# Kernel tuning notes

Hardware: AMD Instinct MI355X
Metric: run time of the kernel (lower is better)

## Reference

```python
import jax, jax.numpy as jnp
import numpy as np

N_NODES = 100000
N_EDGES = 1600000
NEG_SLOPE = 0.01  # F.leaky_relu default


def _param(key, shape, scale=0.05):
    return jax.random.normal(key, shape, dtype=jnp.float32) * scale


def setup_inputs() -> dict:
    key = jax.random.key(0)
    ks = jax.random.split(key, 32)
    inp = {
        "x": jax.random.normal(ks[0], (N_NODES, 64), dtype=jnp.float32),
        "edge_index": jax.random.randint(ks[1], (2, N_EDGES), 0, N_NODES, dtype=jnp.int64),
        # encoder SAGEConv params: lin_l (neighbors, with bias) + lin_r (root)
        "ggn1_Wl": _param(ks[2], (128, 64)), "ggn1_b": jnp.zeros((128,), jnp.float32), "ggn1_Wr": _param(ks[3], (128, 64)),
        "ggn2_Wl": _param(ks[4], (128, 128)), "ggn2_b": jnp.zeros((128,), jnp.float32), "ggn2_Wr": _param(ks[5], (128, 128)),
        "ggn3_Wl": _param(ks[6], (128, 128)), "ggn3_b": jnp.zeros((128,), jnp.float32), "ggn3_Wr": _param(ks[7], (128, 128)),
        "tr2_W": _param(ks[8], (64, 128)), "tr2_b": jnp.zeros((64,), jnp.float32),
        # decoder
        "dec1_W": _param(ks[9], (128, 64)), "dec1_b": jnp.zeros((128,), jnp.float32),
        "dec2_Wl": _param(ks[10], (128, 128)), "dec2_b": jnp.zeros((128,), jnp.float32), "dec2_Wr": _param(ks[11], (128, 128)),
        "dec3_Wl": _param(ks[12], (64, 128)), "dec3_b": jnp.zeros((64,), jnp.float32), "dec3_Wr": _param(ks[13], (64, 128)),
        "dec4_Wl": _param(ks[14], (3, 64)), "dec4_b": jnp.zeros((3,), jnp.float32), "dec4_Wr": _param(ks[15], (3, 64)),
    }
    return inp


def _sage(x, src, dst, Wl, b, Wr, n):
    # PyG SAGEConv (aggr='mean'): lin_l(mean_{j->i} x_j) + lin_r(x_i)
    msgs = x[src]                                              # [E, d] gather
    s = jax.ops.segment_sum(msgs, dst, num_segments=n)          # [N, d]
    cnt = jax.ops.segment_sum(jnp.ones((src.shape[0], 1), x.dtype), dst, num_segments=n)
    mean = s / jnp.maximum(cnt, 1.0)
    return mean @ Wl.T + b + x @ Wr.T


def _leaky(h):
    return jnp.where(h > 0, h, NEG_SLOPE * h)


def reference(x, edge_index,
              ggn1_Wl, ggn1_b, ggn1_Wr,
              ggn2_Wl, ggn2_b, ggn2_Wr,
              ggn3_Wl, ggn3_b, ggn3_Wr,
              tr2_W, tr2_b,
              dec1_W, dec1_b,
              dec2_Wl, dec2_b, dec2_Wr,
              dec3_Wl, dec3_b, dec3_Wr,
              dec4_Wl, dec4_b, dec4_Wr):
    n = x.shape[0]
    src, dst = edge_index[0], edge_index[1]  # source_to_target flow
    # --- encode (dropout = identity, deterministic reference) ---
    h = jnp.tanh(_sage(x, src, dst, ggn1_Wl, ggn1_b, ggn1_Wr, n))
    h = jnp.tanh(_sage(h, src, dst, ggn2_Wl, ggn2_b, ggn2_Wr, n))
    h = jnp.tanh(_sage(h, src, dst, ggn3_Wl, ggn3_b, ggn3_Wr, n))
    mu = h @ tr2_W.T + tr2_b
    logvar = mu  # module applies the same tr2 twice
    z = mu       # reparametrize in eval mode returns mu
    # --- decode ---
    o = _leaky(z @ dec1_W.T + dec1_b)
    o = _leaky(_sage(o, src, dst, dec2_Wl, dec2_b, dec2_Wr, n))
    o = jnp.tanh(_sage(o, src, dst, dec3_Wl, dec3_b, dec3_Wr, n))
    z2 = _sage(o, src, dst, dec4_Wl, dec4_b, dec4_Wr, n)
    return (z2[:, :2], z2[:, 2], mu, logvar)
```

## Files before the change

### kernel.cpp

```cpp
#include <hip/hip_runtime.h>
#include <cmath>


constexpr int ACT_NONE = 0, ACT_TANH = 1, ACT_LEAKY = 2;
constexpr int SCAN_CHUNK = 4096;

typedef __attribute__((ext_vector_type(8))) __bf16 bf16x8;
typedef __attribute__((ext_vector_type(4))) float f32x4;
typedef __attribute__((ext_vector_type(4))) unsigned short u16x4;
typedef __attribute__((ext_vector_type(8))) unsigned short u16x8;

__device__ __forceinline__ unsigned short f2h(float x) {
  _Float16 h = (_Float16)x;
  unsigned short u;
  __builtin_memcpy(&u, &h, 2);
  return u;
}
__device__ __forceinline__ float hlo(unsigned int u) {
  unsigned short s = (unsigned short)(u & 0xffffu);
  _Float16 h;
  __builtin_memcpy(&h, &s, 2);
  return (float)h;
}
__device__ __forceinline__ float hhi(unsigned int u) {
  unsigned short s = (unsigned short)(u >> 16);
  _Float16 h;
  __builtin_memcpy(&h, &s, 2);
  return (float)h;
}
__device__ __forceinline__ void split_bf16(float x, __bf16& h, __bf16& l) {
  h = (__bf16)x;
  l = (__bf16)(x - (float)h);
}
__device__ __forceinline__ unsigned short b2u(__bf16 b) {
  unsigned short u;
  __builtin_memcpy(&u, &b, 2);
  return u;
}

__global__ __launch_bounds__(256) void split_x_kernel(const float* __restrict__ in,
                                                      __bf16* __restrict__ hi,
                                                      __bf16* __restrict__ lo, int total) {
  int i = (blockIdx.x * 256 + threadIdx.x) * 4;
  if (i >= total) return;
  float4 v = *(const float4*)(in + i);
  float vv[4] = {v.x, v.y, v.z, v.w};
  u16x4 h, l;
#pragma unroll
  for (int j = 0; j < 4; ++j) {
    __bf16 hb, lb;
    split_bf16(vv[j], hb, lb);
    h[j] = b2u(hb);
    l[j] = b2u(lb);
  }
  *(u16x4*)(hi + i) = h;
  *(u16x4*)(lo + i) = l;
}

__global__ __launch_bounds__(256) void split_w_kernel(
    const float* p0, const float* p1, const float* p2, const float* p3,
    const float* p4, const float* p5, const float* p6, const float* p7,
    const float* p8, const float* p9, const float* p10, const float* p11,
    __bf16* __restrict__ hi, __bf16* __restrict__ lo) {
  int b = blockIdx.x;
  const float* src;
  int boff, doff;
  if      (b < 8)   { src = p0;  boff = b;       doff = 0; }
  else if (b < 16)  { src = p1;  boff = b - 8;   doff = 8192; }
  else if (b < 32)  { src = p2;  boff = b - 16;  doff = 16384; }
  else if (b < 48)  { src = p3;  boff = b - 32;  doff = 32768; }
  else if (b < 64)  { src = p4;  boff = b - 48;  doff = 49152; }
  else if (b < 80)  { src = p5;  boff = b - 64;  doff = 65536; }
  else if (b < 88)  { src = p6;  boff = b - 80;  doff = 81920; }
  else if (b < 96)  { src = p7;  boff = b - 88;  doff = 90112; }
  else if (b < 112) { src = p8;  boff = b - 96;  doff = 98304; }
  else if (b < 128) { src = p9;  boff = b - 112; doff = 114688; }
  else if (b < 136) { src = p10; boff = b - 128; doff = 131072; }
  else              { src = p11; boff = b - 136; doff = 139264; }
  int i = boff * 1024 + threadIdx.x * 4;
  float4 v = *(const float4*)(src + i);
  float vv[4] = {v.x, v.y, v.z, v.w};
  u16x4 h, l;
#pragma unroll
  for (int j = 0; j < 4; ++j) {
    __bf16 hb, lb;
    split_bf16(vv[j], hb, lb);
    h[j] = b2u(hb);
    l[j] = b2u(lb);
  }
  *(u16x4*)(hi + doff + i) = h;
  *(u16x4*)(lo + doff + i) = l;
}

__global__ __launch_bounds__(256) void count_rank_kernel(const int* __restrict__ dst,
                                                         int* __restrict__ cnt,
                                                         int* __restrict__ rank, int E) {
  int e = blockIdx.x * 256 + threadIdx.x;
  if (e < E) rank[e] = atomicAdd(&cnt[dst[e]], 1);
}

__global__ __launch_bounds__(1024) void scan_blk_kernel(const int* __restrict__ cnt,
                                                        int* __restrict__ rowptr,
                                                        float* __restrict__ inv,
                                                        int* __restrict__ bsum, int n) {
  __shared__ int wsum[17];
  const int lane = threadIdx.x & 63;
  const int wid = threadIdx.x >> 6;
  const int i0 = blockIdx.x * SCAN_CHUNK + threadIdx.x * 4;
  int v[4];
  if (i0 + 3 < n) {
    int4 t = *(const int4*)(cnt + i0);
    v[0] = t.x; v[1] = t.y; v[2] = t.z; v[3] = t.w;
  } else {
#pragma unroll
    for (int j = 0; j < 4; ++j) v[j] = (i0 + j < n) ? cnt[i0 + j] : 0;
  }
#pragma unroll
  for (int j = 0; j < 4; ++j)
    if (i0 + j < n) inv[i0 + j] = 1.0f / (float)(v[j] > 1 ? v[j] : 1);
  const int s = v[0] + v[1] + v[2] + v[3];
  int x = s;
#pragma unroll
  for (int off = 1; off < 64; off <<= 1) {
    int t = __shfl_up(x, off);
    if (lane >= off) x += t;
  }
  if (lane == 63) wsum[wid + 1] = x;
  __syncthreads();
  if (threadIdx.x == 0) {
    wsum[0] = 0;
    for (int w = 1; w <= 16; ++w) wsum[w] += wsum[w - 1];
    bsum[blockIdx.x] = wsum[16];
  }
  __syncthreads();
  int p = wsum[wid] + x - s;
#pragma unroll
  for (int j = 0; j < 4; ++j) {
    if (i0 + j < n) rowptr[i0 + j] = p;
    p += v[j];
  }
}

__global__ __launch_bounds__(1024) void scan_sums_kernel(int* __restrict__ bsum,
                                                         int* __restrict__ rowptr,
                                                         int nb, int n) {
  __shared__ int wsum[17];
  const int lane = threadIdx.x & 63;
  const int wid = threadIdx.x >> 6;
  const int v = (threadIdx.x < nb) ? bsum[threadIdx.x] : 0;
  int x = v;
#pragma unroll
  for (int off = 1; off < 64; off <<= 1) {
    int t = __shfl_up(x, off);
    if (lane >= off) x += t;
  }
  if (lane == 63) wsum[wid + 1] = x;
  __syncthreads();
  if (threadIdx.x == 0) {
    wsum[0] = 0;
    for (int w = 1; w <= 16; ++w) wsum[w] += wsum[w - 1];
    rowptr[n] = wsum[16];
  }
  __syncthreads();
  if (threadIdx.x < nb) bsum[threadIdx.x] = wsum[wid] + x - v;
}

__global__ __launch_bounds__(1024) void scan_add_kernel(int* __restrict__ rowptr,
                                                        const int* __restrict__ bsum,
                                                        int n) {
  const int off = bsum[blockIdx.x];
  const int i0 = blockIdx.x * SCAN_CHUNK + threadIdx.x * 4;
  if (i0 + 3 < n) {
    int4 t = *(const int4*)(rowptr + i0);
    t.x += off; t.y += off; t.z += off; t.w += off;
    *(int4*)(rowptr + i0) = t;
  } else {
    for (int j = 0; j < 4; ++j)
      if (i0 + j < n) rowptr[i0 + j] += off;
  }
}

__global__ __launch_bounds__(256) void scatter_kernel(const int* __restrict__ src,
                                                      const int* __restrict__ dst,
                                                      const int* __restrict__ rowptr,
                                                      const int* __restrict__ rank,
                                                      int* __restrict__ esrc, int E) {
  int e = blockIdx.x * 256 + threadIdx.x;
  if (e < E) esrc[rowptr[dst[e]] + rank[e]] = src[e];
}

__global__ __launch_bounds__(256) void gather_f32s_kernel(
    const float* __restrict__ in, const int* __restrict__ esrc,
    const int* __restrict__ rowptr, const float* __restrict__ inv,
    __bf16* __restrict__ Mhi, __bf16* __restrict__ Mlo, int n) {
  const int node = blockIdx.x * 4 + (threadIdx.x >> 6);
  const int lane = threadIdx.x & 63;
  if (node >= n) return;
  const int beg = rowptr[node];
  const int end = rowptr[node + 1];
  const float iv = inv[node];
  float a0 = 0.f, a1 = 0.f, a2 = 0.f, a3 = 0.f;
  for (int b = beg; b < end; b += 64) {
    int m = end - b;
    if (m > 64) m = 64;
    int myi = (lane < m) ? esrc[b + lane] : 0;
    int s = 0;
    for (; s + 4 <= m; s += 4) {
      int i0 = __shfl(myi, s);
      int i1 = __shfl(myi, s + 1);
      int i2 = __shfl(myi, s + 2);
      int i3 = __shfl(myi, s + 3);
      a0 += in[(size_t)i0 * 64 + lane];
      a1 += in[(size_t)i1 * 64 + lane];
      a2 += in[(size_t)i2 * 64 + lane];
      a3 += in[(size_t)i3 * 64 + lane];
    }
    for (; s < m; ++s) {
      int i0 = __shfl(myi, s);
      a0 += in[(size_t)i0 * 64 + lane];
    }
  }
  float mv = ((a0 + a1) + (a2 + a3)) * iv;
  __bf16 h, l;
  split_bf16(mv, h, l);
  Mhi[(size_t)node * 64 + lane] = h;
  Mlo[(size_t)node * 64 + lane] = l;
}

__global__ __launch_bounds__(256) void gather_s16_kernel(
    const unsigned short* __restrict__ inq, const int* __restrict__ esrc,
    const int* __restrict__ rowptr, const float* __restrict__ inv,
    __bf16* __restrict__ Mhi, __bf16* __restrict__ Mlo, int n) {
  const int node = blockIdx.x * 4 + (threadIdx.x >> 6);
  const int lane = threadIdx.x & 63;
  if (node >= n) return;
  const int beg = rowptr[node];
  const int end = rowptr[node + 1];
  const float iv = inv[node] * (1.0f / 32767.0f);
  const unsigned int* bu = (const unsigned int*)inq;
  int a0l = 0, a0h = 0, a1l = 0, a1h = 0;
  int a2l = 0, a2h = 0, a3l = 0, a3h = 0;
  for (int b = beg; b < end; b += 64) {
    int m = end - b;
    if (m > 64) m = 64;
    int myi = (lane < m) ? esrc[b + lane] : 0;
    int s = 0;
    for (; s + 4 <= m; s += 4) {
      int i0 = __shfl(myi, s);
      int i1 = __shfl(myi, s + 1);
      int i2 = __shfl(myi, s + 2);
      int i3 = __shfl(myi, s + 3);
      unsigned int u0 = bu[(size_t)i0 * 64 + lane];
      unsigned int u1 = bu[(size_t)i1 * 64 + lane];
      unsigned int u2 = bu[(size_t)i2 * 64 + lane];
      unsigned int u3 = bu[(size_t)i3 * 64 + lane];
      a0l += (int)(short)u0; a0h += ((int)u0) >> 16;
      a1l += (int)(short)u1; a1h += ((int)u1) >> 16;
      a2l += (int)(short)u2; a2h += ((int)u2) >> 16;
      a3l += (int)(short)u3; a3h += ((int)u3) >> 16;
    }
    for (; s < m; ++s) {
      int i0 = __shfl(myi, s);
      unsigned int u0 = bu[(size_t)i0 * 64 + lane];
      a0l += (int)(short)u0; a0h += ((int)u0) >> 16;
    }
  }
  float rx = (float)((a0l + a1l) + (a2l + a3l)) * iv;
  float ry = (float)((a0h + a1h) + (a2h + a3h)) * iv;
  __bf16 h0, l0, h1, l1;
  split_bf16(rx, h0, l0);
  split_bf16(ry, h1, l1);
  ((unsigned int*)Mhi)[(size_t)node * 64 + lane] =
      (unsigned int)b2u(h0) | ((unsigned int)b2u(h1) << 16);
  ((unsigned int*)Mlo)[(size_t)node * 64 + lane] =
      (unsigned int)b2u(l0) | ((unsigned int)b2u(l1) << 16);
}

__global__ __launch_bounds__(256) void gather_h128_kernel(
    const unsigned short* __restrict__ inh, const int* __restrict__ esrc,
    const int* __restrict__ rowptr, const float* __restrict__ inv,
    __bf16* __restrict__ Mhi, __bf16* __restrict__ Mlo, int n) {
  const int node = blockIdx.x * 4 + (threadIdx.x >> 6);
  const int lane = threadIdx.x & 63;
  if (node >= n) return;
  const int beg = rowptr[node];
  const int end = rowptr[node + 1];
  const float iv = inv[node];
  const unsigned int* bu = (const unsigned int*)inh;
  float a0x = 0.f, a0y = 0.f, a1x = 0.f, a1y = 0.f;
  float a2x = 0.f, a2y = 0.f, a3x = 0.f, a3y = 0.f;
  for (int b = beg; b < end; b += 64) {
    int m = end - b;
    if (m > 64) m = 64;
    int myi = (lane < m) ? esrc[b + lane] : 0;
    int s = 0;
    for (; s + 4 <= m; s += 4) {
      int i0 = __shfl(myi, s);
      int i1 = __shfl(myi, s + 1);
      int i2 = __shfl(myi, s + 2);
      int i3 = __shfl(myi, s + 3);
      unsigned int u0 = bu[(size_t)i0 * 64 + lane];
      unsigned int u1 = bu[(size_t)i1 * 64 + lane];
      unsigned int u2 = bu[(size_t)i2 * 64 + lane];
      unsigned int u3 = bu[(size_t)i3 * 64 + lane];
      a0x += hlo(u0); a0y += hhi(u0);
      a1x += hlo(u1); a1y += hhi(u1);
      a2x += hlo(u2); a2y += hhi(u2);
      a3x += hlo(u3); a3y += hhi(u3);
    }
    for (; s < m; ++s) {
      int i0 = __shfl(myi, s);
      unsigned int u0 = bu[(size_t)i0 * 64 + lane];
      a0x += hlo(u0); a0y += hhi(u0);
    }
  }
  float rx = ((a0x + a1x) + (a2x + a3x)) * iv;
  float ry = ((a0y + a1y) + (a2y + a3y)) * iv;
  __bf16 h0, l0, h1, l1;
  split_bf16(rx, h0, l0);
  split_bf16(ry, h1, l1);
  ((unsigned int*)Mhi)[(size_t)node * 64 + lane] =
      (unsigned int)b2u(h0) | ((unsigned int)b2u(h1) << 16);
  ((unsigned int*)Mlo)[(size_t)node * 64 + lane] =
      (unsigned int)b2u(l0) | ((unsigned int)b2u(l1) << 16);
}

__global__ __launch_bounds__(256) void gather_h64_kernel(
    const unsigned short* __restrict__ inh, const int* __restrict__ esrc,
    const int* __restrict__ rowptr, const float* __restrict__ inv,
    float* __restrict__ meanb, int n) {
  const int node = blockIdx.x * 4 + (threadIdx.x >> 6);
  const int lane = threadIdx.x & 63;
  if (node >= n) return;
  const int beg = rowptr[node];
  const int end = rowptr[node + 1];
  const float iv = inv[node];
  const unsigned int* bu = (const unsigned int*)inh;
  const int half = lane >> 5;
  const int hl = lane & 31;
  float ax = 0.f, ay = 0.f, bx = 0.f, by = 0.f;
  for (int b = beg; b < end; b += 64) {
    int m = end - b;
    if (m > 64) m = 64;
    int myi = (lane < m) ? esrc[b + lane] : 0;
    int s = 0;
    for (; s + 4 <= m; s += 4) {
      int i0 = __shfl(myi, s + half);
      int i1 = __shfl(myi, s + 2 + half);
      unsigned int u0 = bu[(size_t)i0 * 32 + hl];
      unsigned int u1 = bu[(size_t)i1 * 32 + hl];
      ax += hlo(u0); ay += hhi(u0);
      bx += hlo(u1); by += hhi(u1);
    }
    for (; s < m; s += 2) {
      int t = s + half;
      if (t < m) {
        int i0 = __shfl(myi, t);
        unsigned int u0 = bu[(size_t)i0 * 32 + hl];
        ax += hlo(u0); ay += hhi(u0);
      }
    }
  }
  float sx = ax + bx, sy = ay + by;
  sx += __shfl_xor(sx, 32);
  sy += __shfl_xor(sy, 32);
  if (half == 0)
    ((float2*)meanb)[(size_t)node * 32 + hl] = make_float2(sx * iv, sy * iv);
}

__global__ __launch_bounds__(256) void gather_mean4_kernel(
    const float* __restrict__ y4, const int* __restrict__ esrc,
    const int* __restrict__ rowptr, const float* __restrict__ inv,
    float* __restrict__ mean4, int n) {
  int i = blockIdx.x * 256 + threadIdx.x;
  if (i >= n) return;
  const int beg = rowptr[i], end = rowptr[i + 1];
  const float iv = inv[i];
  float sx = 0.f, sy = 0.f, sz = 0.f;
  const float4* b = (const float4*)y4;
  for (int j = beg; j < end; ++j) {
    float4 v = b[esrc[j]];
    sx += v.x; sy += v.y; sz += v.z;
  }
  ((float4*)mean4)[i] = make_float4(sx * iv, sy * iv, sz * iv, 0.f);
}

template <int DI, int DO, int ACT, bool AGG, bool ADDMEAN, bool BIAS, int SH,
          bool OSPLIT, int ASRC>
__global__ __launch_bounds__(256) void node_mfma_kernel(
    const __bf16* __restrict__ Ahi, const __bf16* __restrict__ Alo,
    const __bf16* __restrict__ Mhi, const __bf16* __restrict__ Mlo,
    const __bf16* __restrict__ Wrhi, const __bf16* __restrict__ Wrlo,
    const __bf16* __restrict__ Wlhi, const __bf16* __restrict__ Wllo,
    const float* __restrict__ bias, const float* __restrict__ meanF,
    float* __restrict__ out, float* __restrict__ out2,
    unsigned short* __restrict__ outh,
    __bf16* __restrict__ ohi, __bf16* __restrict__ olo, int n) {
  constexpr int BM = 128;
  constexpr int KC = 32;
  constexpr int KS = 40;
  constexpr int CT = DO / 16;
  __shared__ __align__(16) __bf16 As_hi[BM * KS];
  __shared__ __align__(16) __bf16 As_lo[BM * KS];
  __shared__ __align__(16) __bf16 Ws_hi[DO * KS];
  __shared__ __align__(16) __bf16 Ws_lo[DO * KS];

  const int wv = threadIdx.x >> 6;
  const int lane = threadIdx.x & 63;
  const int lm = lane & 15;
  const int lq = lane >> 4;
  const int row0 = blockIdx.x * BM;

  f32x4 acc[2][CT];
#pragma unroll
  for (int rt = 0; rt < 2; ++rt)
#pragma unroll
    for (int ct = 0; ct < CT; ++ct) acc[rt][ct] = (f32x4){0.f, 0.f, 0.f, 0.f};

  const int nphase = AGG ? 2 : 1;
  for (int phase = 0; phase < nphase; ++phase) {
    const __bf16* AH = (phase == 0) ? Ahi : Mhi;
    const __bf16* AL = (phase == 0) ? Alo : Mlo;
    const __bf16* WH = (phase == 0) ? Wrhi : Wlhi;
    const __bf16* WL = (phase == 0) ? Wrlo : Wllo;
    for (int k0 = 0; k0 < DI; k0 += KC) {
      {
        const int r = threadIdx.x >> 1;
        const int kb = (threadIdx.x & 1) * 16;
        const int row = row0 + r;
        bf16x8 h0, h1, l0, l1;
        if (ASRC == 2 && phase == 0) {
          u16x8 q0, q1;
          if (row < n) {
            const u16x8* pq =
                (const u16x8*)((const unsigned short*)AH + (size_t)row * DI + k0 + kb);
            q0 = pq[0]; q1 = pq[1];
          } else {
#pragma unroll
            for (int j = 0; j < 8; ++j) { q0[j] = 0; q1[j] = 0; }
          }
#pragma unroll
          for (int j = 0; j < 8; ++j) {
            __bf16 hb, lb;
            split_bf16((float)(short)q0[j] * (1.0f / 32767.0f), hb, lb);
            h0[j] = hb; l0[j] = lb;
            split_bf16((float)(short)q1[j] * (1.0f / 32767.0f), hb, lb);
            h1[j] = hb; l1[j] = lb;
          }
        } else {
          if (row < n) {
            const bf16x8* ph = (const bf16x8*)(AH + (size_t)row * DI + k0 + kb);
            const bf16x8* pl = (const bf16x8*)(AL + (size_t)row * DI + k0 + kb);
            h0 = ph[0]; h1 = ph[1];
            l0 = pl[0]; l1 = pl[1];
          } else {
            bf16x8 z;
#pragma unroll
            for (int j = 0; j < 8; ++j) z[j] = (__bf16)0.f;
            h0 = h1 = l0 = l1 = z;
          }
        }
        *(bf16x8*)(&As_hi[r * KS + kb]) = h0;
        *(bf16x8*)(&As_hi[r * KS + kb + 8]) = h1;
        *(bf16x8*)(&As_lo[r * KS + kb]) = l0;
        *(bf16x8*)(&As_lo[r * KS + kb + 8]) = l1;
      }
      if constexpr (DO == 128) {
        const int c = threadIdx.x >> 1;
        const int kb = (threadIdx.x & 1) * 16;
        const bf16x8* ph = (const bf16x8*)(WH + (size_t)c * DI + k0 + kb);
        const bf16x8* pl = (const bf16x8*)(WL + (size_t)c * DI + k0 + kb);
        *(bf16x8*)(&Ws_hi[c * KS + kb]) = ph[0];
        *(bf16x8*)(&Ws_hi[c * KS + kb + 8]) = ph[1];
        *(bf16x8*)(&Ws_lo[c * KS + kb]) = pl[0];
        *(bf16x8*)(&Ws_lo[c * KS + kb + 8]) = pl[1];
      } else {
        const int c = threadIdx.x >> 2;
        const int kb = (threadIdx.x & 3) * 8;
        *(bf16x8*)(&Ws_hi[c * KS + kb]) =
            *(const bf16x8*)(WH + (size_t)c * DI + k0 + kb);
        *(bf16x8*)(&Ws_lo[c * KS + kb]) =
            *(const bf16x8*)(WL + (size_t)c * DI + k0 + kb);
      }
      __syncthreads();
      const int kb = lq * 8;
      bf16x8 ah[2], al[2];
#pragma unroll
      for (int rt = 0; rt < 2; ++rt) {
        const int r = wv * 32 + rt * 16 + lm;
        ah[rt] = *(const bf16x8*)(&As_hi[r * KS + kb]);
        al[rt] = *(const bf16x8*)(&As_lo[r * KS + kb]);
      }
#pragma unroll
      for (int ct = 0; ct < CT; ++ct) {
        const int c = ct * 16 + lm;
        bf16x8 bh = *(const bf16x8*)(&Ws_hi[c * KS + kb]);
        bf16x8 bl = *(const bf16x8*)(&Ws_lo[c * KS + kb]);
#pragma unroll
        for (int rt = 0; rt < 2; ++rt) {
          acc[rt][ct] = __builtin_amdgcn_mfma_f32_16x16x32_bf16(ah[rt], bh, acc[rt][ct], 0, 0, 0);
          acc[rt][ct] = __builtin_amdgcn_mfma_f32_16x16x32_bf16(al[rt], bh, acc[rt][ct], 0, 0, 0);
          acc[rt][ct] = __builtin_amdgcn_mfma_f32_16x16x32_bf16(ah[rt], bl, acc[rt][ct], 0, 0, 0);
        }
      }
      __syncthreads();
    }
  }

#pragma unroll
  for (int rt = 0; rt < 2; ++rt)
#pragma unroll
    for (int ct = 0; ct < CT; ++ct) {
      const int col = ct * 16 + lm;
      const float bval = BIAS ? bias[col] : 0.f;
      f32x4 a = acc[rt][ct];
#pragma unroll
      for (int r = 0; r < 4; ++r) {
        const int row = row0 + wv * 32 + rt * 16 + lq * 4 + r;
        if (row < n) {
          float t = a[r] + bval;
          if (ADDMEAN) t += meanF[(size_t)row * DO + col];
          if (ACT == ACT_TANH) t = tanhf(t);
          else if (ACT == ACT_LEAKY) t = (t > 0.f) ? t : 0.01f * t;
          if (out) out[(size_t)row * DO + col] = t;
          if (out2) out2[(size_t)row * DO + col] = t;
          if constexpr (SH == 1) {
            if (outh) outh[(size_t)row * DO + col] = f2h(t);
          } else if constexpr (SH == 2) {
            if (outh)
              outh[(size_t)row * DO + col] =
                  (unsigned short)(short)__builtin_rintf(t * 32767.0f);
          }
          if constexpr (OSPLIT) {
            __bf16 hb, lb;
            split_bf16(t, hb, lb);
            ohi[(size_t)row * DO + col] = hb;
            olo[(size_t)row * DO + col] = lb;
          }
        }
      }
    }
}

__global__ __launch_bounds__(256) void dec4_pre_kernel(
    const float* __restrict__ hB, const float* __restrict__ Wl,
    float* __restrict__ y4, int n) {
  const int node = blockIdx.x * 4 + (threadIdx.x >> 6);
  const int lane = threadIdx.x & 63;
  if (node >= n) return;
  float v = hB[(size_t)node * 64 + lane];
  float p0 = v * Wl[lane];
  float p1 = v * Wl[64 + lane];
  float p2 = v * Wl[128 + lane];
#pragma unroll
  for (int off = 32; off >= 1; off >>= 1) {
    p0 += __shfl_xor(p0, off);
    p1 += __shfl_xor(p1, off);
    p2 += __shfl_xor(p2, off);
  }
  if (lane == 0) ((float4*)y4)[node] = make_float4(p0, p1, p2, 0.f);
}

__global__ __launch_bounds__(256) void dec4_final_kernel(
    const float* __restrict__ hB, const float* __restrict__ mean4,
    const float* __restrict__ Wr, const float* __restrict__ bias,
    float* __restrict__ out, int n) {
  const int node = blockIdx.x * 4 + (threadIdx.x >> 6);
  const int lane = threadIdx.x & 63;
  if (node >= n) return;
  float v = hB[(size_t)node * 64 + lane];
  float p0 = v * Wr[lane];
  float p1 = v * Wr[64 + lane];
  float p2 = v * Wr[128 + lane];
#pragma unroll
  for (int off = 32; off >= 1; off >>= 1) {
    p0 += __shfl_xor(p0, off);
    p1 += __shfl_xor(p1, off);
    p2 += __shfl_xor(p2, off);
  }
  if (lane == 0) {
    float4 m = ((const float4*)mean4)[node];
    out[2 * (size_t)node]     = p0 + m.x + bias[0];
    out[2 * (size_t)node + 1] = p1 + m.y + bias[1];
    out[2 * (size_t)n + node] = p2 + m.z + bias[2];
  }
}

extern "C" void kernel_launch(void* const* d_in, const int* in_sizes, int n_in,
                              void* d_out, int out_size, void* d_ws, size_t ws_size,
                              hipStream_t stream) {
  const float* x = (const float*)d_in[0];
  const int* ei = (const int*)d_in[1];
  const int N = in_sizes[0] / 64;
  const int E = in_sizes[1] / 2;
  const int* src = ei;
  const int* dst = ei + E;
  const float* g1Wl = (const float*)d_in[2];
  const float* g1b  = (const float*)d_in[3];
  const float* g1Wr = (const float*)d_in[4];
  const float* g2Wl = (const float*)d_in[5];
  const float* g2b  = (const float*)d_in[6];
  const float* g2Wr = (const float*)d_in[7];
  const float* g3Wl = (const float*)d_in[8];
  const float* g3b  = (const float*)d_in[9];
  const float* g3Wr = (const float*)d_in[10];
  const float* t2W  = (const float*)d_in[11];
  const float* t2b  = (const float*)d_in[12];
  const float* d1W  = (const float*)d_in[13];
  const float* d1b  = (const float*)d_in[14];
  const float* d2Wl = (const float*)d_in[15];
  const float* d2b  = (const float*)d_in[16];
  const float* d2Wr = (const float*)d_in[17];
  const float* d3Wl = (const float*)d_in[18];
  const float* d3b  = (const float*)d_in[19];
  const float* d3Wr = (const float*)d_in[20];
  const float* d4Wl = (const float*)d_in[21];
  const float* d4b  = (const float*)d_in[22];
  const float* d4Wr = (const float*)d_in[23];

  const size_t N64 = (size_t)N * 64;
  const size_t N128 = (size_t)N * 128;

  char* w = (char*)d_ws;
  auto alloc = [&](size_t bytes) {
    char* p = w;
    w += (bytes + 255) & ~(size_t)255;
    return p;
  };
  __bf16* Ahi = (__bf16*)alloc(N128 * 2);
  __bf16* Alo = (__bf16*)alloc(N128 * 2);
  __bf16* Bhi = (__bf16*)alloc(N128 * 2);
  __bf16* Blo = (__bf16*)alloc(N128 * 2);
  float*  meanF = (float*)alloc(N128 * 4);
  __bf16* xhi = (__bf16*)alloc(N64 * 2);
  __bf16* xlo = (__bf16*)alloc(N64 * 2);
  __bf16* Whi = (__bf16*)alloc(147456 * 2);
  __bf16* Wlo = (__bf16*)alloc(147456 * 2);
  int*    cnt = (int*)alloc((size_t)N * 4);
  float*  inv = (float*)alloc((size_t)N * 4);
  int*    rowp = (int*)alloc(((size_t)N + 1) * 4);
  int*    rank = (int*)alloc((size_t)E * 4);
  int*    esrc = (int*)alloc((size_t)E * 4);
  unsigned short* shB = (unsigned short*)alloc(N128 * 2);

  unsigned short* act1 = (unsigned short*)Ahi;
  unsigned short* act2 = (unsigned short*)Alo;

  __bf16* Mhi = (__bf16*)meanF;
  __bf16* Mlo = Mhi + N128;
  int*    bsum = (int*)meanF;
  float*  y4 = meanF;
  float*  mean4 = meanF + 4 * (size_t)N;
  float*  hBf = meanF + N64;
  __bf16* muhi = xhi;
  __bf16* mulo = xlo;
  unsigned short* shC = (unsigned short*)xhi;

  float* out = (float*)d_out;
  float* mu  = out + 3 * (size_t)N;
  float* lv  = mu + 64 * (size_t)N;

  const int NB = (N + 127) / 128;
  const int GB = (N + 3) / 4;
  const int SB = (N + SCAN_CHUNK - 1) / SCAN_CHUNK;

  const __bf16 *W_g1Wl_h = Whi + 0,      *W_g1Wl_l = Wlo + 0;
  const __bf16 *W_g1Wr_h = Whi + 8192,   *W_g1Wr_l = Wlo + 8192;
  const __bf16 *W_g2Wl_h = Whi + 16384,  *W_g2Wl_l = Wlo + 16384;
  const __bf16 *W_g2Wr_h = Whi + 32768,  *W_g2Wr_l = Wlo + 32768;
  const __bf16 *W_g3Wl_h = Whi + 49152,  *W_g3Wl_l = Wlo + 49152;
  const __bf16 *W_g3Wr_h = Whi + 65536,  *W_g3Wr_l = Wlo + 65536;
  const __bf16 *W_t2W_h  = Whi + 81920,  *W_t2W_l  = Wlo + 81920;
  const __bf16 *W_d1W_h  = Whi + 90112,  *W_d1W_l  = Wlo + 90112;
  const __bf16 *W_d2Wl_h = Whi + 98304,  *W_d2Wl_l = Wlo + 98304;
  const __bf16 *W_d2Wr_h = Whi + 114688, *W_d2Wr_l = Wlo + 114688;
  const __bf16 *W_d3Wl_h = Whi + 131072, *W_d3Wl_l = Wlo + 131072;
  const __bf16 *W_d3Wr_h = Whi + 139264, *W_d3Wr_l = Wlo + 139264;

  split_x_kernel<<<(int)((N64 + 1023) / 1024), 256, 0, stream>>>(x, xhi, xlo, (int)N64);
  split_w_kernel<<<144, 256, 0, stream>>>(g1Wl, g1Wr, g2Wl, g2Wr, g3Wl, g3Wr,
                                          t2W, d1W, d2Wl, d2Wr, d3Wl, d3Wr, Whi, Wlo);

  hipMemsetAsync(cnt, 0, (size_t)N * sizeof(int), stream);
  count_rank_kernel<<<(E + 255) / 256, 256, 0, stream>>>(dst, cnt, rank, E);
  scan_blk_kernel<<<SB, 1024, 0, stream>>>(cnt, rowp, inv, bsum, N);
  scan_sums_kernel<<<1, 1024, 0, stream>>>(bsum, rowp, SB, N);
  scan_add_kernel<<<SB, 1024, 0, stream>>>(rowp, bsum, N);
  scatter_kernel<<<(E + 255) / 256, 256, 0, stream>>>(src, dst, rowp, rank, esrc, E);

  gather_f32s_kernel<<<GB, 256, 0, stream>>>(x, esrc, rowp, inv, Mhi, Mlo, N);
  node_mfma_kernel<64, 128, ACT_TANH, true, false, true, 2, false, 0><<<NB, 256, 0, stream>>>(
      xhi, xlo, Mhi, Mlo, W_g1Wr_h, W_g1Wr_l, W_g1Wl_h, W_g1Wl_l, g1b, nullptr,
      nullptr, nullptr, act1, nullptr, nullptr, N);

  gather_s16_kernel<<<GB, 256, 0, stream>>>(act1, esrc, rowp, inv, Mhi, Mlo, N);
  node_mfma_kernel<128, 128, ACT_TANH, true, false, true, 2, false, 2><<<NB, 256, 0, stream>>>(
      (const __bf16*)act1, nullptr, Mhi, Mlo, W_g2Wr_h, W_g2Wr_l, W_g2Wl_h, W_g2Wl_l,
      g2b, nullptr, nullptr, nullptr, act2, nullptr, nullptr, N);

  gather_s16_kernel<<<GB, 256, 0, stream>>>(act2, esrc, rowp, inv, Mhi, Mlo, N);
  node_mfma_kernel<128, 128, ACT_TANH, true, false, true, 2, false, 2><<<NB, 256, 0, stream>>>(
      (const __bf16*)act2, nullptr, Mhi, Mlo, W_g3Wr_h, W_g3Wr_l, W_g3Wl_h, W_g3Wl_l,
      g3b, nullptr, nullptr, nullptr, act1, nullptr, nullptr, N);

  node_mfma_kernel<128, 64, ACT_NONE, false, false, true, 0, true, 2><<<NB, 256, 0, stream>>>(
      (const __bf16*)act1, nullptr, nullptr, nullptr, W_t2W_h, W_t2W_l, nullptr, nullptr,
      t2b, nullptr, mu, lv, nullptr, muhi, mulo, N);

  node_mfma_kernel<64, 128, ACT_LEAKY, false, false, true, 1, true, 0><<<NB, 256, 0, stream>>>(
      muhi, mulo, nullptr, nullptr, W_d1W_h, W_d1W_l, nullptr, nullptr, d1b, nullptr,
      nullptr, nullptr, shB, Bhi, Blo, N);

  gather_h128_kernel<<<GB, 256, 0, stream>>>(shB, esrc, rowp, inv, Mhi, Mlo, N);
  node_mfma_kernel<128, 128, ACT_LEAKY, true, false, true, 0, true, 0><<<NB, 256, 0, stream>>>(
      Bhi, Blo, Mhi, Mlo, W_d2Wr_h, W_d2Wr_l, W_d2Wl_h, W_d2Wl_l, d2b, nullptr,
      nullptr, nullptr, nullptr, Ahi, Alo, N);

  node_mfma_kernel<128, 64, ACT_NONE, false, false, false, 1, false, 0><<<NB, 256, 0, stream>>>(
      Ahi, Alo, nullptr, nullptr, W_d3Wl_h, W_d3Wl_l, nullptr, nullptr, nullptr, nullptr,
      nullptr, nullptr, shC, nullptr, nullptr, N);
  gather_h64_kernel<<<GB, 256, 0, stream>>>(shC, esrc, rowp, inv, meanF, N);
  node_mfma_kernel<128, 64, ACT_TANH, false, true, true, 0, false, 0><<<NB, 256, 0, stream>>>(
      Ahi, Alo, nullptr, nullptr, W_d3Wr_h, W_d3Wr_l, nullptr, nullptr, d3b, meanF,
      hBf, nullptr, nullptr, nullptr, nullptr, N);

  dec4_pre_kernel<<<GB, 256, 0, stream>>>(hBf, d4Wl, y4, N);
  gather_mean4_kernel<<<(N + 255) / 256, 256, 0, stream>>>(y4, esrc, rowp, inv, mean4, N);
  dec4_final_kernel<<<GB, 256, 0, stream>>>(hBf, mean4, d4Wr, d4b, out, N);
}
```

Baseline: 965.9 us.

## Stage full weight matrix in LDS once and load A fragments directly to registers

The node MFMA GEMM kernel now loads the whole weight matrix (hi/lo bf16 split) into shared memory once per phase, instead of one 32-wide K chunk at a time. The A operand is no longer staged through LDS: each lane reads its MFMA fragment straight from global memory into registers. This removes the per-chunk __syncthreads pairs and the LDS round-trip for activations. In exchange, LDS use per block grows with DI, which can lower occupancy, and the direct global loads are less coalesced.

```diff
diff --git a/kernel.cpp b/kernel.cpp
--- a/kernel.cpp
+++ b/kernel.cpp
@@ -397,13 +397,11 @@
     unsigned short* __restrict__ outh,
     __bf16* __restrict__ ohi, __bf16* __restrict__ olo, int n) {
   constexpr int BM = 128;
-  constexpr int KC = 32;
-  constexpr int KS = 40;
+  constexpr int KSW = DI + 8;
   constexpr int CT = DO / 16;
-  __shared__ __align__(16) __bf16 As_hi[BM * KS];
-  __shared__ __align__(16) __bf16 As_lo[BM * KS];
-  __shared__ __align__(16) __bf16 Ws_hi[DO * KS];
-  __shared__ __align__(16) __bf16 Ws_lo[DO * KS];
+  constexpr int EL = DO * DI / 256;
+  __shared__ __align__(16) __bf16 Ws_hi[DO * KSW];
+  __shared__ __align__(16) __bf16 Ws_lo[DO * KSW];
 
   const int wv = threadIdx.x >> 6;
   const int lane = threadIdx.x & 63;
@@ -417,85 +415,70 @@
 #pragma unroll
     for (int ct = 0; ct < CT; ++ct) acc[rt][ct] = (f32x4){0.f, 0.f, 0.f, 0.f};
 
+  bf16x8 zf;
+#pragma unroll
+  for (int j = 0; j < 8; ++j) zf[j] = (__bf16)0.f;
+
+  const int rA0 = row0 + wv * 32 + lm;
+  const int rA1 = rA0 + 16;
+  const bool ok0 = rA0 < n;
+  const bool ok1 = rA1 < n;
+  const int kofs = lq * 8;
+
+  const int sc = (threadIdx.x * EL) / DI;
+  const int sk = (threadIdx.x * EL) % DI;
+
   const int nphase = AGG ? 2 : 1;
   for (int phase = 0; phase < nphase; ++phase) {
+    const __bf16* WH = (phase == 0) ? Wrhi : Wlhi;
+    const __bf16* WL = (phase == 0) ? Wrlo : Wllo;
+    if (phase > 0) __syncthreads();
+#pragma unroll
+    for (int j = 0; j < EL / 8; ++j) {
+      *(bf16x8*)(&Ws_hi[sc * KSW + sk + j * 8]) =
+          *(const bf16x8*)(WH + (size_t)sc * DI + sk + j * 8);
+      *(bf16x8*)(&Ws_lo[sc * KSW + sk + j * 8]) =
+          *(const bf16x8*)(WL + (size_t)sc * DI + sk + j * 8);
+    }
+    __syncthreads();
+
     const __bf16* AH = (phase == 0) ? Ahi : Mhi;
     const __bf16* AL = (phase == 0) ? Alo : Mlo;
-    const __bf16* WH = (phase == 0) ? Wrhi : Wlhi;
-    const __bf16* WL = (phase == 0) ? Wrlo : Wllo;
-    for (int k0 = 0; k0 < DI; k0 += KC) {
-      {
-        const int r = threadIdx.x >> 1;
-        const int kb = (threadIdx.x & 1) * 16;
-        const int row = row0 + r;
-        bf16x8 h0, h1, l0, l1;
-        if (ASRC == 2 && phase == 0) {
-          u16x8 q0, q1;
-          if (row < n) {
-            const u16x8* pq =
-                (const u16x8*)((const unsigned short*)AH + (size_t)row * DI + k0 + kb);
-            q0 = pq[0]; q1 = pq[1];
-          } else {
-#pragma unroll
-            for (int j = 0; j < 8; ++j) { q0[j] = 0; q1[j] = 0; }
-          }
-#pragma unroll
-          for (int j = 0; j < 8; ++j) {
-            __bf16 hb, lb;
-            split_bf16((float)(short)q0[j] * (1.0f / 32767.0f), hb, lb);
-            h0[j] = hb; l0[j] = lb;
-            split_bf16((float)(short)q1[j] * (1.0f / 32767.0f), hb, lb);
-            h1[j] = hb; l1[j] = lb;
-          }
-        } else {
-          if (row < n) {
-            const bf16x8* ph = (const bf16x8*)(AH + (size_t)row * DI + k0 + kb);
-            const bf16x8* pl = (const bf16x8*)(AL + (size_t)row * DI + k0 + kb);
-            h0 = ph[0]; h1 = ph[1];
-            l0 = pl[0]; l1 = pl[1];
-          } else {
-            bf16x8 z;
-#pragma unroll
-            for (int j = 0; j < 8; ++j) z[j] = (__bf16)0.f;
-            h0 = h1 = l0 = l1 = z;
-          }
+#pragma unroll
+    for (int k0 = 0; k0 < DI; k0 += 32) {
+      bf16x8 ah[2], al[2];
+      if (ASRC == 2 && phase == 0) {
+        const unsigned short* Q = (const unsigned short*)AH;
+        u16x8 q0, q1;
+        if (ok0) q0 = *(const u16x8*)(Q + (size_t)rA0 * DI + k0 + kofs);
+        else {
+#pragma unroll
+          for (int j = 0; j < 8; ++j) q0[j] = 0;
         }
-        *(bf16x8*)(&As_hi[r * KS + kb]) = h0;
-        *(bf16x8*)(&As_hi[r * KS + kb + 8]) = h1;
-        *(bf16x8*)(&As_lo[r * KS + kb]) = l0;
-        *(bf16x8*)(&As_lo[r * KS + kb + 8]) = l1;
-      }
-      if constexpr (DO == 128) {
-        const int c = threadIdx.x >> 1;
-        const int kb = (threadIdx.x & 1) * 16;
-        const bf16x8* ph = (const bf16x8*)(WH + (size_t)c * DI + k0 + kb);
-        const bf16x8* pl = (const bf16x8*)(WL + (size_t)c * DI + k0 + kb);
-        *(bf16x8*)(&Ws_hi[c * KS + kb]) = ph[0];
-        *(bf16x8*)(&Ws_hi[c * KS + kb + 8]) = ph[1];
-        *(bf16x8*)(&Ws_lo[c * KS + kb]) = pl[0];
-        *(bf16x8*)(&Ws_lo[c * KS + kb + 8]) = pl[1];
+        if (ok1) q1 = *(const u16x8*)(Q + (size_t)rA1 * DI + k0 + kofs);
+        else {
+#pragma unroll
+          for (int j = 0; j < 8; ++j) q1[j] = 0;
+        }
+#pragma unroll
+        for (int j = 0; j < 8; ++j) {
+          __bf16 hb, lb;
+          split_bf16((float)(short)q0[j] * (1.0f / 32767.0f), hb, lb);
+          ah[0][j] = hb; al[0][j] = lb;
+          split_bf16((float)(short)q1[j] * (1.0f / 32767.0f), hb, lb);
+          ah[1][j] = hb; al[1][j] = lb;
+        }
       } else {
-        const int c = threadIdx.x >> 2;
-        const int kb = (threadIdx.x & 3) * 8;
-        *(bf16x8*)(&Ws_hi[c * KS + kb]) =
-            *(const bf16x8*)(WH + (size_t)c * DI + k0 + kb);
-        *(bf16x8*)(&Ws_lo[c * KS + kb]) =
-            *(const bf16x8*)(WL + (size_t)c * DI + k0 + kb);
-      }
-      __syncthreads();
-      const int kb = lq * 8;
-      bf16x8 ah[2], al[2];
-#pragma unroll
-      for (int rt = 0; rt < 2; ++rt) {
-        const int r = wv * 32 + rt * 16 + lm;
-        ah[rt] = *(const bf16x8*)(&As_hi[r * KS + kb]);
-        al[rt] = *(const bf16x8*)(&As_lo[r * KS + kb]);
+        ah[0] = ok0 ? *(const bf16x8*)(AH + (size_t)rA0 * DI + k0 + kofs) : zf;
+        al[0] = ok0 ? *(const bf16x8*)(AL + (size_t)rA0 * DI + k0 + kofs) : zf;
+        ah[1] = ok1 ? *(const bf16x8*)(AH + (size_t)rA1 * DI + k0 + kofs) : zf;
+        al[1] = ok1 ? *(const bf16x8*)(AL + (size_t)rA1 * DI + k0 + kofs) : zf;
       }
 #pragma unroll
       for (int ct = 0; ct < CT; ++ct) {
         const int c = ct * 16 + lm;
-        bf16x8 bh = *(const bf16x8*)(&Ws_hi[c * KS + kb]);
-        bf16x8 bl = *(const bf16x8*)(&Ws_lo[c * KS + kb]);
+        bf16x8 bh = *(const bf16x8*)(&Ws_hi[c * KSW + k0 + kofs]);
+        bf16x8 bl = *(const bf16x8*)(&Ws_lo[c * KSW + k0 + kofs]);
 #pragma unroll
         for (int rt = 0; rt < 2; ++rt) {
           acc[rt][ct] = __builtin_amdgcn_mfma_f32_16x16x32_bf16(ah[rt], bh, acc[rt][ct], 0, 0, 0);
@@ -503,7 +486,6 @@
           acc[rt][ct] = __builtin_amdgcn_mfma_f32_16x16x32_bf16(ah[rt], bl, acc[rt][ct], 0, 0, 0);
         }
       }
-      __syncthreads();
     }
   }
 
```

After: 973.4 us. Within noise of the previous version (+0.8%).
